# Performance work log

Hardware: AMD Instinct MI355X
Metric: run time of the kernel (lower is better)

Reference implementation:

```python
import jax, jax.numpy as jnp
import numpy as np

N, D = 200000, 256          # num nodes, feature dim
B, NEG = 1024, 64           # batch size, neg_sample_size
S1, S2 = 25, 10             # num_samples for layer 0 and layer 1
OUT = 128                   # per-layer output_dim (concat -> 2*OUT emitted)


def setup_inputs() -> dict:
    key = jax.random.key(0)
    ks = jax.random.split(key, 14)
    inp = {
        "features": jax.random.normal(ks[0], (N, D), jnp.float32),
        "W_self0": jax.random.normal(ks[1], (D, OUT), jnp.float32) / np.sqrt(D).astype(np.float32),
        "W_neigh0": jax.random.normal(ks[2], (D, OUT), jnp.float32) / np.sqrt(D).astype(np.float32),
        "W_self1": jax.random.normal(ks[3], (2 * OUT, OUT), jnp.float32) / np.sqrt(2 * OUT).astype(np.float32),
        "W_neigh1": jax.random.normal(ks[4], (2 * OUT, OUT), jnp.float32) / np.sqrt(2 * OUT).astype(np.float32),
        "s1_0": jax.random.randint(ks[5], (B,), 0, N),
        "s1_1": jax.random.randint(ks[6], (B * S2,), 0, N),
        "s1_2": jax.random.randint(ks[7], (B * S2 * S1,), 0, N),
        "s2_0": jax.random.randint(ks[8], (B,), 0, N),
        "s2_1": jax.random.randint(ks[9], (B * S2,), 0, N),
        "s2_2": jax.random.randint(ks[10], (B * S2 * S1,), 0, N),
        "n_0": jax.random.randint(ks[11], (NEG,), 0, N),
        "n_1": jax.random.randint(ks[12], (NEG * S2,), 0, N),
        "n_2": jax.random.randint(ks[13], (NEG * S2 * S1,), 0, N),
    }
    return inp


def _agg(h_self, h_neigh, Ws, Wn, act):
    """GraphSAGE mean aggregator with concat=True: [M, 2*OUT]."""
    return act(jnp.concatenate([h_self @ Ws, jnp.mean(h_neigh, axis=1) @ Wn], axis=-1))


def _l2norm(x):
    return x / jnp.maximum(jnp.linalg.norm(x, axis=1, keepdims=True), 1e-12)


def reference(features, W_self0, W_neigh0, W_self1, W_neigh1,
              s1_0, s1_1, s1_2, s2_0, s2_1, s2_2, n_0, n_1, n_2):
    def encode(i0, i1, i2, bs):
        h0 = features[i0]                     # [bs, D]
        h1 = features[i1]                     # [bs*S2, D]
        h2 = features[i2]                     # [bs*S2*S1, D]
        # layer 0 (ReLU), applied at hop 0 and hop 1
        g0 = _agg(h0, h1.reshape(bs, S2, D), W_self0, W_neigh0, jax.nn.relu)          # [bs, 2*OUT]
        g1 = _agg(h1, h2.reshape(bs * S2, S1, D), W_self0, W_neigh0, jax.nn.relu)     # [bs*S2, 2*OUT]
        # layer 1 (identity act), hop 0 only
        out = _agg(g0, g1.reshape(bs, S2, 2 * OUT), W_self1, W_neigh1, lambda x: x)   # [bs, 2*OUT]
        return _l2norm(out)

    u1 = encode(s1_0, s1_1, s1_2, B)
    u2 = encode(s2_0, s2_1, s2_2, B)
    un = encode(n_0, n_1, n_2, NEG)

    aff = jnp.sum(u1 * u2, axis=-1)          # [B] positive affinities
    neg_aff = u1 @ un.T                      # [B, NEG]
    # sigmoid cross-entropy: pos label 1, neg label 0
    loss = (jnp.sum(jax.nn.softplus(-aff)) + jnp.sum(jax.nn.softplus(neg_aff))) / B
    return loss, aff, neg_aff, u1
```

## Files before the change

### kernel.cpp

```cpp
#include <hip/hip_runtime.h>
#include <math.h>

#define DD   256
#define BB   1024
#define NEGN 64
#define S1N  25
#define S2N  10
#define OUTN 128
#define NB   (2 * BB + NEGN)
#define NREF1 (2 * BB * S2N + NEGN * S2N)
#define NREF  (NREF1 + NB)
#define NREFP 23280
#define TBLK 1250

typedef unsigned int  uint;
typedef unsigned short ushort;
typedef unsigned char uchar;
typedef short bf16x8 __attribute__((ext_vector_type(8)));
typedef float f32x4  __attribute__((ext_vector_type(4)));
typedef float f32x2  __attribute__((ext_vector_type(2)));

__device__ __forceinline__ ushort f2bf(float x) {
    uint u = __float_as_uint(x);
    u += 0x7FFFu + ((u >> 16) & 1u);
    return (ushort)(u >> 16);
}
__device__ __forceinline__ float bflo(uint v) { return __uint_as_float(v << 16); }
__device__ __forceinline__ float bfhi(uint v) { return __uint_as_float(v & 0xFFFF0000u); }

#if __has_builtin(__builtin_amdgcn_cvt_pk_fp8_f32) && __has_builtin(__builtin_amdgcn_cvt_pk_f32_fp8)
__device__ __forceinline__ uchar fp8_enc(float x) {
    return (uchar)(__builtin_amdgcn_cvt_pk_fp8_f32(x, x, 0, false) & 0xff);
}
template <bool HI>
__device__ __forceinline__ f32x2 fp8_dec2(uint v) {
    return __builtin_amdgcn_cvt_pk_f32_fp8(v, HI);
}
#else
__device__ __forceinline__ uchar fp8_enc(float x) {
    uint u = __float_as_uint(x);
    uint s = (u >> 24) & 0x80u;
    float a = fabsf(x);
    if (a >= 448.f) return (uchar)(s | 0x7Eu);
    if (a < 0.0009765625f) return (uchar)s;
    int e; float fm = frexpf(a, &e);
    int pe = e - 1;
    uint code;
    if (pe >= -6) {
        int mi = (int)rintf((fm * 2.0f - 1.0f) * 8.0f);
        if (mi == 8) { mi = 0; pe += 1; }
        if (pe > 8) return (uchar)(s | 0x7Eu);
        code = ((uint)(pe + 7) << 3) | (uint)mi;
        if (code > 0x7Eu) code = 0x7Eu;
    } else {
        int mi = (int)rintf(a * 512.0f);
        code = (mi >= 8) ? 8u : (uint)mi;
    }
    return (uchar)(s | code);
}
__device__ __forceinline__ float fp8_dec1(uint b) {
    uint s = (b & 0x80u) << 24;
    uint em = b & 0x7fu;
    if (em >= 8) return __uint_as_float(s | ((em + 960u) << 20));
    float v = (float)em * 0.001953125f;
    return (b & 0x80u) ? -v : v;
}
template <bool HI>
__device__ __forceinline__ f32x2 fp8_dec2(uint v) {
    f32x2 r;
    uint w = HI ? (v >> 16) : v;
    r.x = fp8_dec1(w & 0xffu);
    r.y = fp8_dec1((w >> 8) & 0xffu);
    return r;
}
#endif

__global__ __launch_bounds__(256)
void prep_w_k(const float* __restrict__ Ws0, const float* __restrict__ Wn0,
              ushort* __restrict__ Wt) {
    int col = blockIdx.x;
    int k   = threadIdx.x;
    const float* W = (col < OUTN) ? Ws0 : Wn0;
    int j = col & (OUTN - 1);
    Wt[(size_t)col * 256 + k] = f2bf(W[(size_t)k * OUTN + j]);
}

struct SegI {
    const int* i0[3];
    const int* i1[3];
    const int* i2[3];
};

__device__ __forceinline__ int map_ref(int r, const SegI& ix) {
    r = min(r, NREF - 1);
    if (r < 10240) return ix.i1[0][r];
    if (r < 20480) return ix.i1[1][r - 10240];
    if (r < 21120) return ix.i1[2][r - 20480];
    if (r < 22144) return ix.i0[0][r - 21120];
    if (r < 23168) return ix.i0[1][r - 22144];
    return ix.i0[2][r - 23168];
}

__global__ __launch_bounds__(256)
void trans_ysg_k(const float* __restrict__ feat, const ushort* __restrict__ Wt,
                 SegI ix, uchar* __restrict__ yn8, ushort* __restrict__ ysr) {
    __shared__ ushort As[32 * 256];
    int w = threadIdx.x >> 6, l = threadIdx.x & 63;
    int lane16 = l & 15, kb = (l >> 4) * 8;

    if (blockIdx.x < TBLK) {
        int rh = w >> 1, ch = w & 1;
        bf16x8 bfr[4][8];
#pragma unroll
        for (int c = 0; c < 4; ++c) {
            int col = 128 + ch * 64 + c * 16 + lane16;
#pragma unroll
            for (int kk = 0; kk < 8; ++kk)
                bfr[c][kk] = *(const bf16x8*)(Wt + (size_t)col * 256 + kk * 32 + kb);
        }
        int rr = threadIdx.x >> 4;
        int cq = threadIdx.x & 15;

        for (int tile = 0; tile < 5; ++tile) {
            size_t row0 = (size_t)blockIdx.x * 160 + tile * 32;
            uint2 wr[2][4];
#pragma unroll
            for (int hf = 0; hf < 2; ++hf) {
                int r = hf * 16 + rr;
#pragma unroll
                for (int q = 0; q < 4; ++q) {
                    float4 x = *(const float4*)(feat + (row0 + r) * 256 + cq * 16 + q * 4);
                    wr[hf][q].x = (uint)f2bf(x.x) | ((uint)f2bf(x.y) << 16);
                    wr[hf][q].y = (uint)f2bf(x.z) | ((uint)f2bf(x.w) << 16);
                }
            }
            __syncthreads();
#pragma unroll
            for (int hf = 0; hf < 2; ++hf) {
                int r = hf * 16 + rr;
#pragma unroll
                for (int q = 0; q < 4; ++q) {
                    int col = cq * 16 + q * 4;
                    *(uint2*)&As[r * 256 + (col ^ ((r & 7) << 3))] = wr[hf][q];
                }
            }
            __syncthreads();

            f32x4 acc[4];
#pragma unroll
            for (int c = 0; c < 4; ++c)
#pragma unroll
                for (int j = 0; j < 4; ++j) acc[c][j] = 0.f;

            int arow = rh * 16 + lane16;
#pragma unroll
            for (int kk = 0; kk < 8; ++kk) {
                int k0 = kk * 32 + kb;
                bf16x8 af = *(const bf16x8*)&As[arow * 256 + (k0 ^ ((arow & 7) << 3))];
#pragma unroll
                for (int c = 0; c < 4; ++c)
                    acc[c] = __builtin_amdgcn_mfma_f32_16x16x32_bf16(af, bfr[c][kk], acc[c], 0, 0, 0);
            }

#pragma unroll
            for (int c = 0; c < 4; ++c) {
                int col = ch * 64 + c * 16 + lane16;
#pragma unroll
                for (int j = 0; j < 4; ++j) {
                    size_t grow = row0 + rh * 16 + (l >> 4) * 4 + j;
                    yn8[grow * 128 + col] = fp8_enc(acc[c][j]);
                }
            }
        }
    } else {
        int bid = blockIdx.x - TBLK;
        bf16x8 bfr[2][8];
#pragma unroll
        for (int c = 0; c < 2; ++c) {
            int col = w * 32 + c * 16 + lane16;
#pragma unroll
            for (int kk = 0; kk < 8; ++kk)
                bfr[c][kk] = *(const bf16x8*)(Wt + (size_t)col * 256 + kk * 32 + kb);
        }
        int rr = threadIdx.x >> 4;
        int cq = threadIdx.x & 15;

        for (int tile = 0; tile < 5; ++tile) {
            int row0 = bid * 80 + tile * 16;
            int src = map_ref(row0 + rr, ix);
            uint2 wr[4];
#pragma unroll
            for (int q = 0; q < 4; ++q) {
                float4 x = *(const float4*)(feat + (size_t)src * 256 + cq * 16 + q * 4);
                wr[q].x = (uint)f2bf(x.x) | ((uint)f2bf(x.y) << 16);
                wr[q].y = (uint)f2bf(x.z) | ((uint)f2bf(x.w) << 16);
            }
            __syncthreads();
#pragma unroll
            for (int q = 0; q < 4; ++q) {
                int col = cq * 16 + q * 4;
                *(uint2*)&As[rr * 256 + (col ^ ((rr & 7) << 3))] = wr[q];
            }
            __syncthreads();

            f32x4 acc[2];
#pragma unroll
            for (int c = 0; c < 2; ++c)
#pragma unroll
                for (int j = 0; j < 4; ++j) acc[c][j] = 0.f;

#pragma unroll
            for (int kk = 0; kk < 8; ++kk) {
                int k0 = kk * 32 + kb;
                bf16x8 af = *(const bf16x8*)&As[lane16 * 256 + (k0 ^ ((lane16 & 7) << 3))];
#pragma unroll
                for (int c = 0; c < 2; ++c)
                    acc[c] = __builtin_amdgcn_mfma_f32_16x16x32_bf16(af, bfr[c][kk], acc[c], 0, 0, 0);
            }

#pragma unroll
            for (int c = 0; c < 2; ++c) {
                int col = w * 32 + c * 16 + lane16;
#pragma unroll
                for (int j = 0; j < 4; ++j) {
                    size_t grow = (size_t)row0 + (l >> 4) * 4 + j;
                    ysr[grow * 128 + col] = f2bf(acc[c][j]);
                }
            }
        }
    }
}

__global__ __launch_bounds__(320)
void gather_all_k(const uint* __restrict__ ysrp, const uint* __restrict__ yn8u,
                  SegI ix, float* __restrict__ mg1, float* __restrict__ g0) {
    __shared__ float msL[5][64][2];
    __shared__ float mnL[5][32][4];
    __shared__ float gnL[5][32][4];
    int wv = threadIdx.x >> 6;
    int l  = threadIdx.x & 63;
    int b = blockIdx.x;

    int seg, lb;
    if (b < BB) { seg = 0; lb = b; }
    else if (b < 2 * BB) { seg = 1; lb = b - BB; }
    else { seg = 2; lb = b - 2 * BB; }
    const int sbase1[3] = {0, 10240, 20480};
    const int sbase0[3] = {21120, 22144, 23168};
    const int* p1 = ix.i1[seg];
    const int* p2 = ix.i2[seg];

    int i2v = (l < 50) ? p2[(size_t)lb * 250 + wv * 50 + l] : 0;
    int ia = p1[lb * S2N + 2 * wv];
    int ib = p1[lb * S2N + 2 * wv + 1];

    int half = l >> 5;
    int cg   = l & 31;

    float accA[4] = {0.f, 0.f, 0.f, 0.f};
    float accB[4] = {0.f, 0.f, 0.f, 0.f};
#pragma unroll
    for (int p = 0; p < 25; ++p) {
        int rlo = __builtin_amdgcn_readlane(i2v, 2 * p);
        int rhi = __builtin_amdgcn_readlane(i2v, 2 * p + 1);
        int ni = half ? rhi : rlo;
        uint v = yn8u[(size_t)ni * 32 + cg];
        f32x2 f01 = fp8_dec2<false>(v);
        f32x2 f23 = fp8_dec2<true>(v);
        if (p < 12) {
            accA[0] += f01.x; accA[1] += f01.y; accA[2] += f23.x; accA[3] += f23.y;
        } else if (p > 12) {
            accB[0] += f01.x; accB[1] += f01.y; accB[2] += f23.x; accB[3] += f23.y;
        } else {
            if (!half) { accA[0] += f01.x; accA[1] += f01.y; accA[2] += f23.x; accA[3] += f23.y; }
            else       { accB[0] += f01.x; accB[1] += f01.y; accB[2] += f23.x; accB[3] += f23.y; }
        }
    }
    float mnv[4], gnv[4];
    {
        int ng = half ? ib : ia;
        uint v = yn8u[(size_t)ng * 32 + cg];
        f32x2 f01 = fp8_dec2<false>(v);
        f32x2 f23 = fp8_dec2<true>(v);
        gnv[0] = f01.x; gnv[1] = f01.y; gnv[2] = f23.x; gnv[3] = f23.y;
    }
#pragma unroll
    for (int k = 0; k < 4; ++k) {
        accA[k] += __shfl_xor(accA[k], 32, 64);
        accB[k] += __shfl_xor(accB[k], 32, 64);
        gnv[k]  += __shfl_xor(gnv[k], 32, 64);
        mnv[k] = fmaxf(accA[k] * (1.0f / S1N), 0.f) + fmaxf(accB[k] * (1.0f / S1N), 0.f);
    }

    size_t refa = (size_t)(sbase1[seg] + lb * S2N + 2 * wv);
    uint sva = ysrp[refa * 64 + l];
    uint svb = ysrp[(refa + 1) * 64 + l];
    float ms0 = fmaxf(bflo(sva), 0.f) + fmaxf(bflo(svb), 0.f);
    float ms1 = fmaxf(bfhi(sva), 0.f) + fmaxf(bfhi(svb), 0.f);

    msL[wv][l][0] = ms0; msL[wv][l][1] = ms1;
    if (l < 32) {
#pragma unroll
        for (int k = 0; k < 4; ++k) { mnL[wv][l][k] = mnv[k]; gnL[wv][l][k] = gnv[k]; }
    }
    __syncthreads();

    int g = threadIdx.x >> 6, c = l;
    const float invS2 = 1.0f / S2N;
    if (g == 0) {
        float s0 = 0.f, s1 = 0.f;
#pragma unroll
        for (int w2 = 0; w2 < 5; ++w2) { s0 += msL[w2][c][0]; s1 += msL[w2][c][1]; }
        float2 o; o.x = s0 * invS2; o.y = s1 * invS2;
        *(float2*)(mg1 + (size_t)b * DD + 2 * c) = o;
    } else if (g == 1) {
        if (c < 32) {
            float4 o;
            float s[4] = {0.f, 0.f, 0.f, 0.f};
#pragma unroll
            for (int w2 = 0; w2 < 5; ++w2)
#pragma unroll
                for (int k = 0; k < 4; ++k) s[k] += mnL[w2][c][k];
            o.x = s[0] * invS2; o.y = s[1] * invS2; o.z = s[2] * invS2; o.w = s[3] * invS2;
            *(float4*)(mg1 + (size_t)b * DD + 128 + 4 * c) = o;
        }
    } else if (g == 2) {
        if (c < 32) {
            float4 o;
            float s[4] = {0.f, 0.f, 0.f, 0.f};
#pragma unroll
            for (int w2 = 0; w2 < 5; ++w2)
#pragma unroll
                for (int k = 0; k < 4; ++k) s[k] += gnL[w2][c][k];
            o.x = fmaxf(s[0] * invS2, 0.f); o.y = fmaxf(s[1] * invS2, 0.f);
            o.z = fmaxf(s[2] * invS2, 0.f); o.w = fmaxf(s[3] * invS2, 0.f);
            *(float4*)(g0 + (size_t)b * DD + 128 + 4 * c) = o;
        }
    } else if (g == 3) {
        uint v = ysrp[(size_t)(sbase0[seg] + lb) * 64 + c];
        float2 o; o.x = fmaxf(bflo(v), 0.f); o.y = fmaxf(bfhi(v), 0.f);
        *(float2*)(g0 + (size_t)b * DD + 2 * c) = o;
    }
}

__global__ __launch_bounds__(256)
void final_fused_k(const float* __restrict__ g0, const float* __restrict__ mg1,
                   const float* __restrict__ Ws, const float* __restrict__ Wn,
                   float* __restrict__ u1, float* __restrict__ u2,
                   float* __restrict__ un) {
    constexpr int R = 8;
    __shared__ float xsS[R][DD];
    __shared__ float xnS[R][DD];
    __shared__ float nrmS[R];
    int r0 = blockIdx.x * R;
    int wv = threadIdx.x >> 6;
    int c  = threadIdx.x & 63;

#pragma unroll
    for (int rr = 0; rr < R / 4; ++rr) {
        int r = wv * (R / 4) + rr;
        int row = r0 + r;
        *(float4*)&xsS[r][c * 4] = *(const float4*)(g0 + (size_t)row * DD + c * 4);
        *(float4*)&xnS[r][c * 4] = *(const float4*)(mg1 + (size_t)row * DD + c * 4);
    }
    __syncthreads();

    int j = threadIdx.x & (OUTN - 1);
    const float* Wj = ((threadIdx.x < OUTN) ? Ws : Wn) + j;
    const float (*X)[DD] = (threadIdx.x < OUTN) ? xsS : xnS;
    float acc[R];
#pragma unroll
    for (int r = 0; r < R; ++r) acc[r] = 0.f;
#pragma unroll 4
    for (int k4 = 0; k4 < DD; k4 += 4) {
        float w0 = Wj[(k4 + 0) * OUTN];
        float w1 = Wj[(k4 + 1) * OUTN];
        float w2 = Wj[(k4 + 2) * OUTN];
        float w3 = Wj[(k4 + 3) * OUTN];
#pragma unroll
        for (int r = 0; r < R; ++r) {
            float4 x = *(const float4*)&X[r][k4];
            acc[r] = fmaf(x.x, w0, acc[r]);
            acc[r] = fmaf(x.y, w1, acc[r]);
            acc[r] = fmaf(x.z, w2, acc[r]);
            acc[r] = fmaf(x.w, w3, acc[r]);
        }
    }
    __syncthreads();
    float* sq = &xsS[0][0];
#pragma unroll
    for (int r = 0; r < R; ++r) sq[r * DD + threadIdx.x] = acc[r] * acc[r];
    __syncthreads();
    {
        int g = threadIdx.x >> 5, ll = threadIdx.x & 31;
        float s = 0.f;
#pragma unroll
        for (int i = 0; i < 8; ++i) s += sq[g * DD + ll + 32 * i];
        s += __shfl_down(s, 16, 64);
        s += __shfl_down(s, 8, 64);
        s += __shfl_down(s, 4, 64);
        s += __shfl_down(s, 2, 64);
        s += __shfl_down(s, 1, 64);
        if (ll == 0) nrmS[g] = fmaxf(sqrtf(s), 1e-12f);
    }
    __syncthreads();
#pragma unroll
    for (int r = 0; r < R; ++r) {
        int row = r0 + r;
        float* dst;
        if (row < BB) dst = u1 + (size_t)row * DD;
        else if (row < 2 * BB) dst = u2 + (size_t)(row - BB) * DD;
        else dst = un + (size_t)(row - 2 * BB) * DD;
        dst[threadIdx.x] = acc[r] / nrmS[r];
    }
}

__device__ __forceinline__ float softplus_f(float x) {
    return fmaxf(x, 0.f) + log1pf(expf(-fabsf(x)));
}

__global__ __launch_bounds__(256)
void aff_neg_k(const float* __restrict__ u1, const float* __restrict__ u2,
               const float* __restrict__ un, float* __restrict__ aff,
               float* __restrict__ neg, float* __restrict__ part) {
    __shared__ float u1s[DD];
    __shared__ float red[256];
    int b = blockIdx.x, t = threadIdx.x;
    float av = u1[(size_t)b * DD + t];
    u1s[t] = av;
    red[t] = av * u2[(size_t)b * DD + t];
    __syncthreads();
    for (int s = 128; s > 0; s >>= 1) { if (t < s) red[t] += red[t + s]; __syncthreads(); }
    float affv = red[0];
    __syncthreads();
    if (t == 0) aff[b] = affv;

    int j = t >> 2, q = t & 3;
    float acc = 0.f;
    const float* up = un + (size_t)j * DD + q * 64;
    const float* us = u1s + q * 64;
#pragma unroll
    for (int i = 0; i < 16; ++i) {
        float4 x = *(const float4*)(up + 4 * i);
        float4 y = *(const float4*)(us + 4 * i);
        acc = fmaf(x.x, y.x, acc); acc = fmaf(x.y, y.y, acc);
        acc = fmaf(x.z, y.z, acc); acc = fmaf(x.w, y.w, acc);
    }
    acc += __shfl_down(acc, 2, 64);
    acc += __shfl_down(acc, 1, 64);
    float sp = 0.f;
    if (q == 0) {
        neg[(size_t)b * NEGN + j] = acc;
        sp = softplus_f(acc);
    }
    if (t == 0) sp += softplus_f(-affv);
    red[t] = sp;
    __syncthreads();
    for (int s = 128; s > 0; s >>= 1) { if (t < s) red[t] += red[t + s]; __syncthreads(); }
    if (t == 0) part[b] = red[0];
}

__global__ __launch_bounds__(256)
void loss_final_k(const float* __restrict__ part, float* __restrict__ loss) {
    __shared__ float red[256];
    int t = threadIdx.x;
    red[t] = part[t] + part[t + 256] + part[t + 512] + part[t + 768];
    __syncthreads();
    for (int s = 128; s > 0; s >>= 1) { if (t < s) red[t] += red[t + s]; __syncthreads(); }
    if (t == 0) loss[0] = red[0] / (float)BB;
}

extern "C" void kernel_launch(void* const* d_in, const int* in_sizes, int n_in,
                              void* d_out, int out_size, void* d_ws, size_t ws_size,
                              hipStream_t stream) {
    const float* feat = (const float*)d_in[0];
    const float* Ws0  = (const float*)d_in[1];
    const float* Wn0  = (const float*)d_in[2];
    const float* Ws1  = (const float*)d_in[3];
    const float* Wn1  = (const float*)d_in[4];
    const int* s1_0 = (const int*)d_in[5];
    const int* s1_1 = (const int*)d_in[6];
    const int* s1_2 = (const int*)d_in[7];
    const int* s2_0 = (const int*)d_in[8];
    const int* s2_1 = (const int*)d_in[9];
    const int* s2_2 = (const int*)d_in[10];
    const int* n_0  = (const int*)d_in[11];
    const int* n_1  = (const int*)d_in[12];
    const int* n_2  = (const int*)d_in[13];

    float* out  = (float*)d_out;
    float* loss = out;
    float* aff  = out + 1;
    float* neg  = out + 1 + BB;
    float* u1   = out + 1 + BB + BB * NEGN;

    char* wsb = (char*)d_ws;
    size_t off = 0;
    ushort* Wt  = (ushort*)(wsb + off); off += (size_t)256 * 256 * 2;
    uchar*  yn8 = (uchar*)(wsb + off);  off += (size_t)200000 * 128;
    ushort* ysr = (ushort*)(wsb + off); off += (size_t)NREFP * 128 * 2;
    float* mg1  = (float*)(wsb + off); off += (size_t)NB * DD * 4;
    float* g0   = (float*)(wsb + off); off += (size_t)NB * DD * 4;
    float* u2   = (float*)(wsb + off); off += (size_t)BB * DD * 4;
    float* un   = (float*)(wsb + off); off += (size_t)NEGN * DD * 4;
    float* part = (float*)(wsb + off); off += (size_t)BB * 4;

    SegI ix;
    ix.i0[0] = s1_0; ix.i0[1] = s2_0; ix.i0[2] = n_0;
    ix.i1[0] = s1_1; ix.i1[1] = s2_1; ix.i1[2] = n_1;
    ix.i2[0] = s1_2; ix.i2[1] = s2_2; ix.i2[2] = n_2;

    prep_w_k<<<256, 256, 0, stream>>>(Ws0, Wn0, Wt);
    trans_ysg_k<<<TBLK + 291, 256, 0, stream>>>(feat, Wt, ix, yn8, ysr);

    gather_all_k<<<NB, 320, 0, stream>>>((const uint*)ysr, (const uint*)yn8, ix, mg1, g0);

    final_fused_k<<<NB / 8, 256, 0, stream>>>(g0, mg1, Ws1, Wn1, u1, u2, un);

    aff_neg_k<<<BB, 256, 0, stream>>>(u1, u2, un, aff, neg, part);
    loss_final_k<<<1, 256, 0, stream>>>(part, loss);
}
```

Measured before the change: 111.3 us.

## Prefetch next feature tile in registers and halve per-warp B fragments in transform kernel

The transform branch now loads and converts the next 32-row feature tile into registers while MFMAs run on the current tile in shared memory, so global loads overlap compute instead of sitting at the top of each iteration. Each warp now covers all 32 rows against 32 output columns (2x2 MFMA tiles) rather than 16 rows against 64 columns, which halves the resident B-fragment registers. Launch bounds now request 4 blocks per CU. The aim is to hide feature-read latency and raise occupancy; the prefetch adds live registers, which partly offsets the savings from the smaller B fragments.

```diff
diff --git a/kernel.cpp b/kernel.cpp
--- a/kernel.cpp
+++ b/kernel.cpp
@@ -101,7 +101,7 @@
     return ix.i0[2][r - 23168];
 }
 
-__global__ __launch_bounds__(256)
+__global__ __launch_bounds__(256, 4)
 void trans_ysg_k(const float* __restrict__ feat, const ushort* __restrict__ Wt,
                  SegI ix, uchar* __restrict__ yn8, ushort* __restrict__ ysr) {
     __shared__ ushort As[32 * 256];
@@ -109,11 +109,11 @@
     int lane16 = l & 15, kb = (l >> 4) * 8;
 
     if (blockIdx.x < TBLK) {
-        int rh = w >> 1, ch = w & 1;
-        bf16x8 bfr[4][8];
-#pragma unroll
-        for (int c = 0; c < 4; ++c) {
-            int col = 128 + ch * 64 + c * 16 + lane16;
+        int cbase = w * 32;
+        bf16x8 bfr[2][8];
+#pragma unroll
+        for (int c = 0; c < 2; ++c) {
+            int col = 128 + cbase + c * 16 + lane16;
 #pragma unroll
             for (int kk = 0; kk < 8; ++kk)
                 bfr[c][kk] = *(const bf16x8*)(Wt + (size_t)col * 256 + kk * 32 + kb);
@@ -121,19 +121,20 @@
         int rr = threadIdx.x >> 4;
         int cq = threadIdx.x & 15;
 
+        uint2 wr[2][4];
+#pragma unroll
+        for (int hf = 0; hf < 2; ++hf) {
+            int r = hf * 16 + rr;
+#pragma unroll
+            for (int q = 0; q < 4; ++q) {
+                float4 x = *(const float4*)(feat + ((size_t)blockIdx.x * 160 + r) * 256 + cq * 16 + q * 4);
+                wr[hf][q].x = (uint)f2bf(x.x) | ((uint)f2bf(x.y) << 16);
+                wr[hf][q].y = (uint)f2bf(x.z) | ((uint)f2bf(x.w) << 16);
+            }
+        }
+
         for (int tile = 0; tile < 5; ++tile) {
-            size_t row0 = (size_t)blockIdx.x * 160 + tile * 32;
-            uint2 wr[2][4];
-#pragma unroll
-            for (int hf = 0; hf < 2; ++hf) {
-                int r = hf * 16 + rr;
-#pragma unroll
-                for (int q = 0; q < 4; ++q) {
-                    float4 x = *(const float4*)(feat + (row0 + r) * 256 + cq * 16 + q * 4);
-                    wr[hf][q].x = (uint)f2bf(x.x) | ((uint)f2bf(x.y) << 16);
-                    wr[hf][q].y = (uint)f2bf(x.z) | ((uint)f2bf(x.w) << 16);
-                }
-            }
+            size_t orow = (size_t)blockIdx.x * 160 + tile * 32;
             __syncthreads();
 #pragma unroll
             for (int hf = 0; hf < 2; ++hf) {
@@ -146,29 +147,50 @@
             }
             __syncthreads();
 
-            f32x4 acc[4];
-#pragma unroll
-            for (int c = 0; c < 4; ++c)
-#pragma unroll
-                for (int j = 0; j < 4; ++j) acc[c][j] = 0.f;
-
-            int arow = rh * 16 + lane16;
+            if (tile < 4) {
+#pragma unroll
+                for (int hf = 0; hf < 2; ++hf) {
+                    int r = hf * 16 + rr;
+#pragma unroll
+                    for (int q = 0; q < 4; ++q) {
+                        float4 x = *(const float4*)(feat + (orow + 32 + r) * 256 + cq * 16 + q * 4);
+                        wr[hf][q].x = (uint)f2bf(x.x) | ((uint)f2bf(x.y) << 16);
+                        wr[hf][q].y = (uint)f2bf(x.z) | ((uint)f2bf(x.w) << 16);
+                    }
+                }
+            }
+
+            f32x4 acc[2][2];
+#pragma unroll
+            for (int rf = 0; rf < 2; ++rf)
+#pragma unroll
+                for (int c = 0; c < 2; ++c)
+#pragma unroll
+                    for (int j = 0; j < 4; ++j) acc[rf][c][j] = 0.f;
+
 #pragma unroll
             for (int kk = 0; kk < 8; ++kk) {
                 int k0 = kk * 32 + kb;
-                bf16x8 af = *(const bf16x8*)&As[arow * 256 + (k0 ^ ((arow & 7) << 3))];
-#pragma unroll
-                for (int c = 0; c < 4; ++c)
-                    acc[c] = __builtin_amdgcn_mfma_f32_16x16x32_bf16(af, bfr[c][kk], acc[c], 0, 0, 0);
-            }
-
-#pragma unroll
-            for (int c = 0; c < 4; ++c) {
-                int col = ch * 64 + c * 16 + lane16;
-#pragma unroll
-                for (int j = 0; j < 4; ++j) {
-                    size_t grow = row0 + rh * 16 + (l >> 4) * 4 + j;
-                    yn8[grow * 128 + col] = fp8_enc(acc[c][j]);
+#pragma unroll
+                for (int rf = 0; rf < 2; ++rf) {
+                    int arow = rf * 16 + lane16;
+                    bf16x8 af = *(const bf16x8*)&As[arow * 256 + (k0 ^ ((arow & 7) << 3))];
+#pragma unroll
+                    for (int c = 0; c < 2; ++c)
+                        acc[rf][c] = __builtin_amdgcn_mfma_f32_16x16x32_bf16(af, bfr[c][kk], acc[rf][c], 0, 0, 0);
+                }
+            }
+
+#pragma unroll
+            for (int rf = 0; rf < 2; ++rf) {
+#pragma unroll
+                for (int c = 0; c < 2; ++c) {
+                    int col = cbase + c * 16 + lane16;
+#pragma unroll
+                    for (int j = 0; j < 4; ++j) {
+                        size_t grow = orow + rf * 16 + (l >> 4) * 4 + j;
+                        yn8[grow * 128 + col] = fp8_enc(acc[rf][c][j]);
+                    }
                 }
             }
         }
```

New measurement: 108.9 us, median of 2. 1.02x faster.

## Stage fp32 rows via async global-to-LDS loads, double-buffer, fold loss into atomics

Applied to the files above, without the earlier changes.

The projection kernel now copies raw fp32 feature rows straight into shared memory with global_load_lds, using a double buffer so the next tile's load overlaps the current tile's MFMA work. Rows are converted to bf16 when fragments are read from LDS, using a packed convert instruction. Both block types now share one 16-row tile shape with 2 column groups per wave, and the launch bounds ask for higher occupancy. Separately, the final loss-reduction kernel is removed: the loss is zeroed in an earlier kernel and each aff_neg block adds its share atomically, which makes the loss summation order nondeterministic.

```diff
diff --git a/kernel.cpp b/kernel.cpp
--- a/kernel.cpp
+++ b/kernel.cpp
@@ -27,6 +27,19 @@
 }
 __device__ __forceinline__ float bflo(uint v) { return __uint_as_float(v << 16); }
 __device__ __forceinline__ float bfhi(uint v) { return __uint_as_float(v & 0xFFFF0000u); }
+
+__device__ __forceinline__ uint cvtpk_bf16(float lo, float hi) {
+    uint r;
+    asm("v_cvt_pk_bf16_f32 %0, %1, %2" : "=v"(r) : "v"(lo), "v"(hi));
+    return r;
+}
+
+__device__ __forceinline__ void load_lds16(const float* g, float* lds) {
+    __builtin_amdgcn_global_load_lds(
+        (const __attribute__((address_space(1))) void*)g,
+        (__attribute__((address_space(3))) void*)lds,
+        16, 0, 0);
+}
 
 #if __has_builtin(__builtin_amdgcn_cvt_pk_fp8_f32) && __has_builtin(__builtin_amdgcn_cvt_pk_f32_fp8)
 __device__ __forceinline__ uchar fp8_enc(float x) {
@@ -101,129 +114,89 @@
     return ix.i0[2][r - 23168];
 }
 
-__global__ __launch_bounds__(256)
+__device__ __forceinline__ bf16x8 lds_frag(const float* As, int r, int k0) {
+    int v = (r & 7) << 2;
+    f32x4 a = *(const f32x4*)(As + r * 256 + ((k0) ^ v));
+    f32x4 b = *(const f32x4*)(As + r * 256 + ((k0 + 4) ^ v));
+    union { uint u[4]; bf16x8 v8; } o;
+    o.u[0] = cvtpk_bf16(a[0], a[1]);
+    o.u[1] = cvtpk_bf16(a[2], a[3]);
+    o.u[2] = cvtpk_bf16(b[0], b[1]);
+    o.u[3] = cvtpk_bf16(b[2], b[3]);
+    return o.v8;
+}
+
+__global__ __launch_bounds__(256, 4)
 void trans_ysg_k(const float* __restrict__ feat, const ushort* __restrict__ Wt,
                  SegI ix, uchar* __restrict__ yn8, ushort* __restrict__ ysr) {
-    __shared__ ushort As[32 * 256];
+    __shared__ __align__(16) float As[2][16 * 256];
     int w = threadIdx.x >> 6, l = threadIdx.x & 63;
     int lane16 = l & 15, kb = (l >> 4) * 8;
 
-    if (blockIdx.x < TBLK) {
-        int rh = w >> 1, ch = w & 1;
-        bf16x8 bfr[4][8];
-#pragma unroll
-        for (int c = 0; c < 4; ++c) {
-            int col = 128 + ch * 64 + c * 16 + lane16;
-#pragma unroll
-            for (int kk = 0; kk < 8; ++kk)
-                bfr[c][kk] = *(const bf16x8*)(Wt + (size_t)col * 256 + kk * 32 + kb);
-        }
-        int rr = threadIdx.x >> 4;
-        int cq = threadIdx.x & 15;
-
-        for (int tile = 0; tile < 5; ++tile) {
-            size_t row0 = (size_t)blockIdx.x * 160 + tile * 32;
-            uint2 wr[2][4];
-#pragma unroll
-            for (int hf = 0; hf < 2; ++hf) {
-                int r = hf * 16 + rr;
-#pragma unroll
-                for (int q = 0; q < 4; ++q) {
-                    float4 x = *(const float4*)(feat + (row0 + r) * 256 + cq * 16 + q * 4);
-                    wr[hf][q].x = (uint)f2bf(x.x) | ((uint)f2bf(x.y) << 16);
-                    wr[hf][q].y = (uint)f2bf(x.z) | ((uint)f2bf(x.w) << 16);
-                }
-            }
-            __syncthreads();
-#pragma unroll
-            for (int hf = 0; hf < 2; ++hf) {
-                int r = hf * 16 + rr;
-#pragma unroll
-                for (int q = 0; q < 4; ++q) {
-                    int col = cq * 16 + q * 4;
-                    *(uint2*)&As[r * 256 + (col ^ ((r & 7) << 3))] = wr[hf][q];
-                }
-            }
-            __syncthreads();
-
-            f32x4 acc[4];
-#pragma unroll
-            for (int c = 0; c < 4; ++c)
-#pragma unroll
-                for (int j = 0; j < 4; ++j) acc[c][j] = 0.f;
-
-            int arow = rh * 16 + lane16;
-#pragma unroll
-            for (int kk = 0; kk < 8; ++kk) {
-                int k0 = kk * 32 + kb;
-                bf16x8 af = *(const bf16x8*)&As[arow * 256 + (k0 ^ ((arow & 7) << 3))];
-#pragma unroll
-                for (int c = 0; c < 4; ++c)
-                    acc[c] = __builtin_amdgcn_mfma_f32_16x16x32_bf16(af, bfr[c][kk], acc[c], 0, 0, 0);
-            }
-
-#pragma unroll
-            for (int c = 0; c < 4; ++c) {
-                int col = ch * 64 + c * 16 + lane16;
+    bool isyn = blockIdx.x < TBLK;
+    int bid = isyn ? blockIdx.x : (blockIdx.x - TBLK);
+    int ntile = isyn ? 10 : 5;
+
+    bf16x8 bfr[2][8];
+    int colbase = (isyn ? 128 : 0) + w * 32;
+#pragma unroll
+    for (int c = 0; c < 2; ++c)
+#pragma unroll
+        for (int kk = 0; kk < 8; ++kk)
+            bfr[c][kk] = *(const bf16x8*)(Wt + (size_t)(colbase + c * 16 + lane16) * 256 + kk * 32 + kb);
+
+    int srcoff4 = ((l * 16) ^ 0) >> 2;
+
+    auto stage = [&](int tile, int buf) {
+#pragma unroll
+        for (int i = 0; i < 4; ++i) {
+            int r = w * 4 + i;
+            int rowg;
+            if (isyn) rowg = bid * 160 + tile * 16 + r;
+            else      rowg = map_ref(bid * 80 + tile * 16 + r, ix);
+            int so = ((l * 16) ^ ((r & 7) << 4)) >> 2;
+            load_lds16(feat + (size_t)rowg * 256 + so, &As[buf][r * 256]);
+        }
+    };
+    (void)srcoff4;
+
+    stage(0, 0);
+    for (int tile = 0; tile < ntile; ++tile) {
+        int buf = tile & 1;
+        __syncthreads();
+        if (tile + 1 < ntile) stage(tile + 1, buf ^ 1);
+
+        f32x4 acc[2];
+#pragma unroll
+        for (int c = 0; c < 2; ++c)
+#pragma unroll
+            for (int j = 0; j < 4; ++j) acc[c][j] = 0.f;
+
+#pragma unroll
+        for (int kk = 0; kk < 8; ++kk) {
+            bf16x8 af = lds_frag(As[buf], lane16, kk * 32 + kb);
+#pragma unroll
+            for (int c = 0; c < 2; ++c)
+                acc[c] = __builtin_amdgcn_mfma_f32_16x16x32_bf16(af, bfr[c][kk], acc[c], 0, 0, 0);
+        }
+
+        if (isyn) {
+#pragma unroll
+            for (int c = 0; c < 2; ++c) {
+                int col = w * 32 + c * 16 + lane16;
 #pragma unroll
                 for (int j = 0; j < 4; ++j) {
-                    size_t grow = row0 + rh * 16 + (l >> 4) * 4 + j;
+                    size_t grow = (size_t)bid * 160 + tile * 16 + (l >> 4) * 4 + j;
                     yn8[grow * 128 + col] = fp8_enc(acc[c][j]);
                 }
             }
-        }
-    } else {
-        int bid = blockIdx.x - TBLK;
-        bf16x8 bfr[2][8];
-#pragma unroll
-        for (int c = 0; c < 2; ++c) {
-            int col = w * 32 + c * 16 + lane16;
-#pragma unroll
-            for (int kk = 0; kk < 8; ++kk)
-                bfr[c][kk] = *(const bf16x8*)(Wt + (size_t)col * 256 + kk * 32 + kb);
-        }
-        int rr = threadIdx.x >> 4;
-        int cq = threadIdx.x & 15;
-
-        for (int tile = 0; tile < 5; ++tile) {
-            int row0 = bid * 80 + tile * 16;
-            int src = map_ref(row0 + rr, ix);
-            uint2 wr[4];
-#pragma unroll
-            for (int q = 0; q < 4; ++q) {
-                float4 x = *(const float4*)(feat + (size_t)src * 256 + cq * 16 + q * 4);
-                wr[q].x = (uint)f2bf(x.x) | ((uint)f2bf(x.y) << 16);
-                wr[q].y = (uint)f2bf(x.z) | ((uint)f2bf(x.w) << 16);
-            }
-            __syncthreads();
-#pragma unroll
-            for (int q = 0; q < 4; ++q) {
-                int col = cq * 16 + q * 4;
-                *(uint2*)&As[rr * 256 + (col ^ ((rr & 7) << 3))] = wr[q];
-            }
-            __syncthreads();
-
-            f32x4 acc[2];
-#pragma unroll
-            for (int c = 0; c < 2; ++c)
-#pragma unroll
-                for (int j = 0; j < 4; ++j) acc[c][j] = 0.f;
-
-#pragma unroll
-            for (int kk = 0; kk < 8; ++kk) {
-                int k0 = kk * 32 + kb;
-                bf16x8 af = *(const bf16x8*)&As[lane16 * 256 + (k0 ^ ((lane16 & 7) << 3))];
-#pragma unroll
-                for (int c = 0; c < 2; ++c)
-                    acc[c] = __builtin_amdgcn_mfma_f32_16x16x32_bf16(af, bfr[c][kk], acc[c], 0, 0, 0);
-            }
-
+        } else {
 #pragma unroll
             for (int c = 0; c < 2; ++c) {
                 int col = w * 32 + c * 16 + lane16;
 #pragma unroll
                 for (int j = 0; j < 4; ++j) {
-                    size_t grow = (size_t)row0 + (l >> 4) * 4 + j;
+                    size_t grow = (size_t)bid * 80 + tile * 16 + (l >> 4) * 4 + j;
                     ysr[grow * 128 + col] = f2bf(acc[c][j]);
                 }
             }
@@ -347,11 +320,12 @@
 void final_fused_k(const float* __restrict__ g0, const float* __restrict__ mg1,
                    const float* __restrict__ Ws, const float* __restrict__ Wn,
                    float* __restrict__ u1, float* __restrict__ u2,
-                   float* __restrict__ un) {
+                   float* __restrict__ un, float* __restrict__ loss) {
     constexpr int R = 8;
     __shared__ float xsS[R][DD];
     __shared__ float xnS[R][DD];
     __shared__ float nrmS[R];
+    if (blockIdx.x == 0 && threadIdx.x == 0) loss[0] = 0.f;
     int r0 = blockIdx.x * R;
     int wv = threadIdx.x >> 6;
     int c  = threadIdx.x & 63;
@@ -422,7 +396,7 @@
 __global__ __launch_bounds__(256)
 void aff_neg_k(const float* __restrict__ u1, const float* __restrict__ u2,
                const float* __restrict__ un, float* __restrict__ aff,
-               float* __restrict__ neg, float* __restrict__ part) {
+               float* __restrict__ neg, float* __restrict__ loss) {
     __shared__ float u1s[DD];
     __shared__ float red[256];
     int b = blockIdx.x, t = threadIdx.x;
@@ -457,17 +431,7 @@
     red[t] = sp;
     __syncthreads();
     for (int s = 128; s > 0; s >>= 1) { if (t < s) red[t] += red[t + s]; __syncthreads(); }
-    if (t == 0) part[b] = red[0];
-}
-
-__global__ __launch_bounds__(256)
-void loss_final_k(const float* __restrict__ part, float* __restrict__ loss) {
-    __shared__ float red[256];
-    int t = threadIdx.x;
-    red[t] = part[t] + part[t + 256] + part[t + 512] + part[t + 768];
-    __syncthreads();
-    for (int s = 128; s > 0; s >>= 1) { if (t < s) red[t] += red[t + s]; __syncthreads(); }
-    if (t == 0) loss[0] = red[0] / (float)BB;
+    if (t == 0) atomicAdd(loss, red[0] * (1.0f / BB));
 }
 
 extern "C" void kernel_launch(void* const* d_in, const int* in_sizes, int n_in,
@@ -503,7 +467,6 @@
     float* g0   = (float*)(wsb + off); off += (size_t)NB * DD * 4;
     float* u2   = (float*)(wsb + off); off += (size_t)BB * DD * 4;
     float* un   = (float*)(wsb + off); off += (size_t)NEGN * DD * 4;
-    float* part = (float*)(wsb + off); off += (size_t)BB * 4;
 
     SegI ix;
     ix.i0[0] = s1_0; ix.i0[1] = s2_0; ix.i0[2] = n_0;
@@ -515,8 +478,7 @@
 
     gather_all_k<<<NB, 320, 0, stream>>>((const uint*)ysr, (const uint*)yn8, ix, mg1, g0);
 
-    final_fused_k<<<NB / 8, 256, 0, stream>>>(g0, mg1, Ws1, Wn1, u1, u2, un);
-
-    aff_neg_k<<<BB, 256, 0, stream>>>(u1, u2, un, aff, neg, part);
-    loss_final_k<<<1, 256, 0, stream>>>(part, loss);
-}
+    final_fused_k<<<NB / 8, 256, 0, stream>>>(g0, mg1, Ws1, Wn1, u1, u2, un, loss);
+
+    aff_neg_k<<<BB, 256, 0, stream>>>(u1, u2, un, aff, neg, loss);
+}
```

Result: slower. 113.9 us (+2.3%).
